# Kernel optimization log

Hardware: AMD Instinct MI355X
Metric: run time of the kernel (lower is better)

The kernel has to match this reference:

```python
import jax, jax.numpy as jnp
import numpy as np

B, H, F, E, K = 32, 4096, 4096, 8, 2

def setup_inputs() -> dict:
    key = jax.random.key(0)
    ks = jax.random.split(key, 5)
    x = jax.random.normal(ks[0], (B, H), dtype=jnp.float32)
    Wg = jax.random.normal(ks[1], (H, E), dtype=jnp.float32) * 0.02
    W1 = jax.random.normal(ks[2], (E, H, F), dtype=jnp.float32) * 0.02
    W3 = jax.random.normal(ks[3], (E, H, F), dtype=jnp.float32) * 0.02
    W2 = jax.random.normal(ks[4], (E, F, H), dtype=jnp.float32) * 0.02
    return {"x": x, "Wg": Wg, "W1": W1, "W3": W3, "W2": W2}

def reference(x, Wg, W1, W3, W2):
    # Gate: [B, E] logits, top-2 selection, softmax over the 2 selected logits
    logits = x @ Wg                                   # [B, E]
    vals, idx = jax.lax.top_k(logits, K)              # [B, K]
    w = jax.nn.softmax(vals, axis=-1)                 # [B, K]
    # Combine weights per expert: [B, E] (zero for unselected experts)
    combine = jnp.sum(jax.nn.one_hot(idx, E, dtype=x.dtype) * w[..., None], axis=1)
    h = jnp.einsum('bh,ehf->ebf', x, W1)              # [E, B, F]
    g = jax.nn.silu(h) * jnp.einsum('bh,ehf->ebf', x, W3)
    y = jnp.einsum('ebf,efh->ebh', g, W2)             # [E, B, H]
    # Scatter-combine: weighted sum over experts (all-gather + reduce-sum in source)
    return jnp.einsum('be,ebh->bh', combine, y)       # [B, H]
```

## Files before the change

kernel.cpp:

```cpp
#include <hip/hip_runtime.h>
#include <cstdint>

#define BB 32
#define HH 4096
#define FF 4096
#define EE 8
#define NSLOT 16
#define TSEG 16

__global__ __launch_bounds__(256) void gate_kernel(const float* __restrict__ x,
                                                   const float* __restrict__ Wg,
                                                   float* __restrict__ logits) {
  int b = blockIdx.x;
  int tid = threadIdx.x;
  float acc[EE];
#pragma unroll
  for (int e = 0; e < EE; ++e) acc[e] = 0.f;
  const float* xb = x + (size_t)b * HH;
  for (int h = tid; h < HH; h += 256) {
    float xv = xb[h];
    const float4* wg = (const float4*)(Wg + (size_t)h * EE);
    float4 w0 = wg[0], w1 = wg[1];
    acc[0] = fmaf(xv, w0.x, acc[0]);
    acc[1] = fmaf(xv, w0.y, acc[1]);
    acc[2] = fmaf(xv, w0.z, acc[2]);
    acc[3] = fmaf(xv, w0.w, acc[3]);
    acc[4] = fmaf(xv, w1.x, acc[4]);
    acc[5] = fmaf(xv, w1.y, acc[5]);
    acc[6] = fmaf(xv, w1.z, acc[6]);
    acc[7] = fmaf(xv, w1.w, acc[7]);
  }
#pragma unroll
  for (int off = 32; off > 0; off >>= 1) {
#pragma unroll
    for (int e = 0; e < EE; ++e) acc[e] += __shfl_down(acc[e], off, 64);
  }
  __shared__ float part[4][EE];
  if ((tid & 63) == 0) {
#pragma unroll
    for (int e = 0; e < EE; ++e) part[tid >> 6][e] = acc[e];
  }
  __syncthreads();
  if (tid < EE) {
    logits[(size_t)b * EE + tid] =
        part[0][tid] + part[1][tid] + part[2][tid] + part[3][tid];
  }
}

__global__ void route_kernel(const float* __restrict__ logits,
                             int* __restrict__ cnt,
                             int* __restrict__ tok,
                             float* __restrict__ wts,
                             int* __restrict__ ord) {
  if (threadIdx.x != 0 || blockIdx.x != 0) return;
  int e0[BB], e1[BB];
  float p0[BB], p1[BB];
  for (int b = 0; b < BB; ++b) {
    const float* L = logits + (size_t)b * EE;
    int i0 = 0;
    float v0 = L[0];
    for (int e = 1; e < EE; ++e) {
      float v = L[e];
      if (v > v0) { v0 = v; i0 = e; }
    }
    int i1 = (i0 == 0) ? 1 : 0;
    float v1 = L[i1];
    for (int e = 0; e < EE; ++e) {
      if (e == i0) continue;
      float v = L[e];
      if (v > v1) { v1 = v; i1 = e; }
    }
    float p = 1.f / (1.f + __expf(v1 - v0));
    e0[b] = i0; e1[b] = i1; p0[b] = p; p1[b] = 1.f - p;
  }
  for (int s = 0; s < NSLOT; ++s) {
    cnt[s] = 0;
    for (int t = 0; t < TSEG; ++t) { tok[s * TSEG + t] = 0; wts[s * TSEG + t] = 0.f; }
  }
  for (int e = 0; e < EE; ++e) {
    int c = 0;
    for (int b = 0; b < BB; ++b) {
      float w = 0.f;
      int sel = 0;
      if (e0[b] == e) { w = p0[b]; sel = 1; }
      else if (e1[b] == e) { w = p1[b]; sel = 1; }
      if (sel) {
        int s = e * 2 + (c >> 4);
        int t = c & 15;
        tok[s * TSEG + t] = b;
        wts[s * TSEG + t] = w;
        cnt[s] = t + 1;
        ++c;
      }
    }
  }
  int na = 0;
  for (int s = 0; s < NSLOT; ++s) if (cnt[s] > 0) ord[na++] = s;
  for (int s = 0; s < NSLOT; ++s) if (cnt[s] == 0) ord[na++] = s;
}

__global__ __launch_bounds__(256) void buildx_kernel(const float* __restrict__ x,
                                                     const int* __restrict__ cnt,
                                                     const int* __restrict__ tok,
                                                     float* __restrict__ xseg) {
  int s = blockIdx.y;
  int c = cnt[s];
  if (c == 0) return;
  int tid = threadIdx.x;
  int t = tid & 15;
  int hoff = tid >> 4;
  int tk = tok[s * TSEG + t];
  bool act = t < c;
  int hbase = blockIdx.x * 256;
#pragma unroll
  for (int i = 0; i < 16; ++i) {
    int h = hbase + i * 16 + hoff;
    float v = act ? x[(size_t)tk * HH + h] : 0.f;
    xseg[((size_t)s * HH + h) * TSEG + t] = v;
  }
}

template <int NT>
__device__ __forceinline__ void fma_row2(float2* __restrict__ acc,
                                         const float* __restrict__ xr, float2 wv) {
  float xs[NT];
#pragma unroll
  for (int q = 0; q < NT; q += 4) *(float4*)&xs[q] = *(const float4*)(xr + q);
#pragma unroll
  for (int t = 0; t < NT; ++t) {
    acc[t].x = fmaf(xs[t], wv.x, acc[t].x);
    acc[t].y = fmaf(xs[t], wv.y, acc[t].y);
  }
}

template <int NT>
__device__ __forceinline__ void accum256_f2(float2* __restrict__ acc,
                                            const float* __restrict__ wp,
                                            const float* __restrict__ xr) {
  float2 ring[16];
#pragma unroll
  for (int k = 0; k < 16; ++k) ring[k] = *(const float2*)(wp + (size_t)k * 4096);
  for (int i0 = 0; i0 + 16 < 256; i0 += 16) {
#pragma unroll
    for (int k = 0; k < 16; ++k) {
      float2 wv = ring[k];
      ring[k] = *(const float2*)(wp + (size_t)(i0 + 16 + k) * 4096);
      fma_row2<NT>(acc, xr + (size_t)(i0 + k) * NT, wv);
    }
  }
#pragma unroll
  for (int k = 0; k < 16; ++k)
    fma_row2<NT>(acc, xr + (size_t)(240 + k) * NT, ring[k]);
}

template <int NT>
__device__ __forceinline__ void stageT(float* __restrict__ lx,
                                       const float* __restrict__ src, int tid) {
  const float4* s4 = (const float4*)src;
  float4* d4 = (float4*)lx;
#pragma unroll
  for (int k = 0; k < NT; ++k) {
    int q = k * 256 + tid;
    int row = q / (NT / 4);
    int part = q & ((NT / 4) - 1);
    d4[q] = s4[row * 4 + part];
  }
}

template <int NT>
__device__ __forceinline__ void stage_silu(float* __restrict__ lx,
                                           const float* __restrict__ h1p,
                                           const float* __restrict__ h3p, int tid) {
  const float4* a4 = (const float4*)h1p;
  const float4* b4 = (const float4*)h3p;
  float4* d4 = (float4*)lx;
#pragma unroll
  for (int k = 0; k < NT; ++k) {
    int q = k * 256 + tid;
    int row = q / (NT / 4);
    int part = q & ((NT / 4) - 1);
    float4 a = a4[row * 4 + part];
    float4 b = b4[row * 4 + part];
    float4 g;
    g.x = (a.x / (1.f + __expf(-a.x))) * b.x;
    g.y = (a.y / (1.f + __expf(-a.y))) * b.y;
    g.z = (a.z / (1.f + __expf(-a.z))) * b.z;
    g.w = (a.w / (1.f + __expf(-a.w))) * b.w;
    d4[q] = g;
  }
}

template <int NT>
__device__ __forceinline__ void passB_body(const float* __restrict__ Wm,
                                           const float* __restrict__ xsrc,
                                           float* __restrict__ segbase,
                                           float* __restrict__ lx, int tid) {
  int l = tid & 63;
  int w = tid >> 6;
  float2 acc[NT];
#pragma unroll
  for (int t = 0; t < NT; ++t) acc[t] = make_float2(0.f, 0.f);
  for (int ch = 0; ch < 4; ++ch) {
    __syncthreads();
    stageT<NT>(lx, xsrc + (size_t)(ch * 1024) * TSEG, tid);
    __syncthreads();
    accum256_f2<NT>(acc, Wm + (size_t)(ch * 1024 + w * 256) * FF + 2 * l,
                    lx + (size_t)(w * 256) * NT);
  }
  __syncthreads();
  float2* red = (float2*)lx;
#pragma unroll
  for (int t = 0; t < NT; ++t) red[(t * 4 + w) * 64 + l] = acc[t];
  __syncthreads();
  constexpr int TH = NT / 2;
  int col_off = tid & 127;
  int half = tid >> 7;
  int lp = col_off >> 1;
  int comp = col_off & 1;
  float v[TH];
#pragma unroll
  for (int j = 0; j < TH; ++j) {
    int t = half * TH + j;
    float sum = 0.f;
#pragma unroll
    for (int w4 = 0; w4 < 4; ++w4)
      sum += lx[(((t * 4 + w4) * 64 + lp) << 1) + comp];
    v[j] = sum;
  }
  float* seg = segbase + (size_t)col_off * TSEG + half * TH;
#pragma unroll
  for (int q = 0; q < TH; q += 4) *(float4*)(seg + q) = *(const float4*)&v[q];
}

__global__ __launch_bounds__(256) void passB6_kernel(const float* __restrict__ W1,
                                                     const float* __restrict__ W3,
                                                     const float* __restrict__ xseg,
                                                     float* __restrict__ h1seg,
                                                     float* __restrict__ h3seg,
                                                     const int* __restrict__ cnt,
                                                     const int* __restrict__ ord) {
  __shared__ float lx[1024 * TSEG];
  int gy = blockIdx.y;
  int s = ord[gy >> 1];
  int mat = gy & 1;
  int c = cnt[s];
  if (c == 0) return;
  int e = s >> 1;
  int colbase = blockIdx.x * 128;
  const float* Wm = (mat ? W3 : W1) + (size_t)e * HH * FF + colbase;
  const float* xsrc = xseg + (size_t)s * HH * TSEG;
  float* segbase = (mat ? h3seg : h1seg) + ((size_t)s * FF + colbase) * TSEG;
  if (c <= 8)
    passB_body<8>(Wm, xsrc, segbase, lx, threadIdx.x);
  else
    passB_body<16>(Wm, xsrc, segbase, lx, threadIdx.x);
}

template <int NT>
__device__ __forceinline__ void passC_body(const float* __restrict__ Wm,
                                           const float* __restrict__ h1src,
                                           const float* __restrict__ h3src,
                                           float* __restrict__ out,
                                           const int* __restrict__ stok,
                                           const float* __restrict__ swt,
                                           int c, int colbase,
                                           float* __restrict__ lx, int tid) {
  int l = tid & 63;
  int w = tid >> 6;
  float2 acc[NT];
#pragma unroll
  for (int t = 0; t < NT; ++t) acc[t] = make_float2(0.f, 0.f);
  for (int ch = 0; ch < 2; ++ch) {
    __syncthreads();
    stage_silu<NT>(lx, h1src + (size_t)(ch * 1024) * TSEG,
                   h3src + (size_t)(ch * 1024) * TSEG, tid);
    __syncthreads();
    accum256_f2<NT>(acc, Wm + (size_t)(ch * 1024 + w * 256) * HH + 2 * l,
                    lx + (size_t)(w * 256) * NT);
  }
  __syncthreads();
  float2* red = (float2*)lx;
#pragma unroll
  for (int t = 0; t < NT; ++t) red[(t * 4 + w) * 64 + l] = acc[t];
  __syncthreads();
  constexpr int TH = NT / 2;
  int col_off = tid & 127;
  int half = tid >> 7;
  int lp = col_off >> 1;
  int comp = col_off & 1;
  float* op = out + colbase + col_off;
#pragma unroll
  for (int j = 0; j < TH; ++j) {
    int t = half * TH + j;
    if (t < c) {
      float sum = 0.f;
#pragma unroll
      for (int w4 = 0; w4 < 4; ++w4)
        sum += lx[(((t * 4 + w4) * 64 + lp) << 1) + comp];
      atomicAdd(op + (size_t)stok[t] * HH, swt[t] * sum);
    }
  }
}

__global__ __launch_bounds__(256) void passC6_kernel(const float* __restrict__ W2,
                                                     const float* __restrict__ h1seg,
                                                     const float* __restrict__ h3seg,
                                                     const int* __restrict__ cnt,
                                                     const int* __restrict__ tok,
                                                     const float* __restrict__ wts,
                                                     const int* __restrict__ ord,
                                                     float* __restrict__ out) {
  __shared__ float lx[1024 * TSEG];
  __shared__ int stok[TSEG];
  __shared__ float swt[TSEG];
  int gy = blockIdx.y;
  int s = ord[gy >> 1];
  int z = gy & 1;
  int c = cnt[s];
  if (c == 0) return;
  int e = s >> 1;
  int colbase = blockIdx.x * 128;
  if (threadIdx.x < TSEG) {
    stok[threadIdx.x] = tok[s * TSEG + threadIdx.x];
    swt[threadIdx.x] = wts[s * TSEG + threadIdx.x];
  }
  const float* Wm = W2 + (size_t)e * FF * HH + (size_t)(z * 2048) * HH + colbase;
  const float* h1src = h1seg + ((size_t)s * FF + z * 2048) * TSEG;
  const float* h3src = h3seg + ((size_t)s * FF + z * 2048) * TSEG;
  if (c <= 8)
    passC_body<8>(Wm, h1src, h3src, out, stok, swt, c, colbase, lx, threadIdx.x);
  else
    passC_body<16>(Wm, h1src, h3src, out, stok, swt, c, colbase, lx, threadIdx.x);
}

extern "C" void kernel_launch(void* const* d_in, const int* in_sizes, int n_in,
                              void* d_out, int out_size, void* d_ws, size_t ws_size,
                              hipStream_t stream) {
  const float* x  = (const float*)d_in[0];
  const float* Wg = (const float*)d_in[1];
  const float* W1 = (const float*)d_in[2];
  const float* W3 = (const float*)d_in[3];
  const float* W2 = (const float*)d_in[4];
  float* out = (float*)d_out;

  char* ws = (char*)d_ws;
  float* logits = (float*)ws;
  int*   cnt    = (int*)(ws + 1024);
  int*   tok    = (int*)(ws + 1088);
  float* wts    = (float*)(ws + 2112);
  int*   ord    = (int*)(ws + 3136);
  float* xseg   = (float*)(ws + 4096);
  float* h1seg  = xseg + (size_t)NSLOT * HH * TSEG;
  float* h3seg  = h1seg + (size_t)NSLOT * FF * TSEG;

  hipMemsetAsync(d_out, 0, (size_t)out_size * sizeof(float), stream);
  gate_kernel<<<BB, 256, 0, stream>>>(x, Wg, logits);
  route_kernel<<<1, 64, 0, stream>>>(logits, cnt, tok, wts, ord);
  buildx_kernel<<<dim3(HH / 256, NSLOT), 256, 0, stream>>>(x, cnt, tok, xseg);
  passB6_kernel<<<dim3(FF / 128, NSLOT * 2), 256, 0, stream>>>(W1, W3, xseg, h1seg, h3seg, cnt, ord);
  passC6_kernel<<<dim3(HH / 128, NSLOT * 2), 256, 0, stream>>>(W2, h1seg, h3seg, cnt, tok, wts, ord, out);
}
```

Measured before the change: 403.2 us.

## Retile expert GEMV passes to float4 weight loads and split token halves

Rewrites the W1/W3 and W2 passes so each thread loads float4 (4 columns) of weights and handles 8 tokens, with lanes split into two token halves. Staging chunks shrink from 1024 to 512 rows, so LDS use drops and more blocks can be resident per CU. The cross-wave reduction now goes through a padded LDS layout (stride 36) to avoid bank conflicts. The c<=8 specialization is dropped, so slots with few tokens now always compute 16 token lanes, but the wider weight loads are meant to improve memory throughput on this bandwidth-bound workload.

```diff
diff --git a/kernel.cpp b/kernel.cpp
--- a/kernel.cpp
+++ b/kernel.cpp
@@ -7,6 +7,8 @@
 #define EE 8
 #define NSLOT 16
 #define TSEG 16
+#define CH 512
+#define RSTR 36
 
 __global__ __launch_bounds__(256) void gate_kernel(const float* __restrict__ x,
                                                    const float* __restrict__ Wg,
@@ -120,189 +122,143 @@
   }
 }
 
-template <int NT>
-__device__ __forceinline__ void fma_row2(float2* __restrict__ acc,
-                                         const float* __restrict__ xr, float2 wv) {
-  float xs[NT];
-#pragma unroll
-  for (int q = 0; q < NT; q += 4) *(float4*)&xs[q] = *(const float4*)(xr + q);
-#pragma unroll
-  for (int t = 0; t < NT; ++t) {
+__device__ __forceinline__ void fma8(float4* __restrict__ acc,
+                                     const float* __restrict__ xr, float4 wv) {
+  float xs[8];
+  *(float4*)&xs[0] = *(const float4*)(xr);
+  *(float4*)&xs[4] = *(const float4*)(xr + 4);
+#pragma unroll
+  for (int t = 0; t < 8; ++t) {
     acc[t].x = fmaf(xs[t], wv.x, acc[t].x);
     acc[t].y = fmaf(xs[t], wv.y, acc[t].y);
-  }
-}
-
-template <int NT>
-__device__ __forceinline__ void accum256_f2(float2* __restrict__ acc,
-                                            const float* __restrict__ wp,
-                                            const float* __restrict__ xr) {
-  float2 ring[16];
-#pragma unroll
-  for (int k = 0; k < 16; ++k) ring[k] = *(const float2*)(wp + (size_t)k * 4096);
-  for (int i0 = 0; i0 + 16 < 256; i0 += 16) {
-#pragma unroll
-    for (int k = 0; k < 16; ++k) {
-      float2 wv = ring[k];
-      ring[k] = *(const float2*)(wp + (size_t)(i0 + 16 + k) * 4096);
-      fma_row2<NT>(acc, xr + (size_t)(i0 + k) * NT, wv);
+    acc[t].z = fmaf(xs[t], wv.z, acc[t].z);
+    acc[t].w = fmaf(xs[t], wv.w, acc[t].w);
+  }
+}
+
+__device__ __forceinline__ void accum128(float4* __restrict__ acc,
+                                         const float4* __restrict__ wp4,
+                                         const float* __restrict__ lxw,
+                                         int half8) {
+  float4 ring[8];
+#pragma unroll
+  for (int k = 0; k < 8; ++k) ring[k] = wp4[(size_t)k * 1024];
+  for (int i0 = 0; i0 + 8 < 128; i0 += 8) {
+#pragma unroll
+    for (int k = 0; k < 8; ++k) {
+      float4 wv = ring[k];
+      ring[k] = wp4[(size_t)(i0 + 8 + k) * 1024];
+      fma8(acc, lxw + (i0 + k) * TSEG + half8, wv);
     }
   }
 #pragma unroll
-  for (int k = 0; k < 16; ++k)
-    fma_row2<NT>(acc, xr + (size_t)(240 + k) * NT, ring[k]);
-}
-
-template <int NT>
-__device__ __forceinline__ void stageT(float* __restrict__ lx,
-                                       const float* __restrict__ src, int tid) {
+  for (int k = 0; k < 8; ++k)
+    fma8(acc, lxw + (120 + k) * TSEG + half8, ring[k]);
+}
+
+__device__ __forceinline__ void stage512(float* __restrict__ lx,
+                                         const float* __restrict__ src, int tid) {
   const float4* s4 = (const float4*)src;
   float4* d4 = (float4*)lx;
 #pragma unroll
-  for (int k = 0; k < NT; ++k) {
-    int q = k * 256 + tid;
-    int row = q / (NT / 4);
-    int part = q & ((NT / 4) - 1);
-    d4[q] = s4[row * 4 + part];
-  }
-}
-
-template <int NT>
-__device__ __forceinline__ void stage_silu(float* __restrict__ lx,
-                                           const float* __restrict__ h1p,
-                                           const float* __restrict__ h3p, int tid) {
+  for (int k = 0; k < 8; ++k) d4[k * 256 + tid] = s4[k * 256 + tid];
+}
+
+__device__ __forceinline__ void stage_silu512(float* __restrict__ lx,
+                                              const float* __restrict__ h1p,
+                                              const float* __restrict__ h3p, int tid) {
   const float4* a4 = (const float4*)h1p;
   const float4* b4 = (const float4*)h3p;
   float4* d4 = (float4*)lx;
 #pragma unroll
-  for (int k = 0; k < NT; ++k) {
-    int q = k * 256 + tid;
-    int row = q / (NT / 4);
-    int part = q & ((NT / 4) - 1);
-    float4 a = a4[row * 4 + part];
-    float4 b = b4[row * 4 + part];
+  for (int k = 0; k < 8; ++k) {
+    float4 a = a4[k * 256 + tid];
+    float4 b = b4[k * 256 + tid];
     float4 g;
     g.x = (a.x / (1.f + __expf(-a.x))) * b.x;
     g.y = (a.y / (1.f + __expf(-a.y))) * b.y;
     g.z = (a.z / (1.f + __expf(-a.z))) * b.z;
     g.w = (a.w / (1.f + __expf(-a.w))) * b.w;
-    d4[q] = g;
-  }
-}
-
-template <int NT>
-__device__ __forceinline__ void passB_body(const float* __restrict__ Wm,
-                                           const float* __restrict__ xsrc,
-                                           float* __restrict__ segbase,
-                                           float* __restrict__ lx, int tid) {
+    d4[k * 256 + tid] = g;
+  }
+}
+
+__device__ __forceinline__ void red_write(float* __restrict__ lds,
+                                          const float4* __restrict__ acc, int tid) {
   int l = tid & 63;
   int w = tid >> 6;
-  float2 acc[NT];
-#pragma unroll
-  for (int t = 0; t < NT; ++t) acc[t] = make_float2(0.f, 0.f);
-  for (int ch = 0; ch < 4; ++ch) {
-    __syncthreads();
-    stageT<NT>(lx, xsrc + (size_t)(ch * 1024) * TSEG, tid);
-    __syncthreads();
-    accum256_f2<NT>(acc, Wm + (size_t)(ch * 1024 + w * 256) * FF + 2 * l,
-                    lx + (size_t)(w * 256) * NT);
-  }
-  __syncthreads();
-  float2* red = (float2*)lx;
-#pragma unroll
-  for (int t = 0; t < NT; ++t) red[(t * 4 + w) * 64 + l] = acc[t];
-  __syncthreads();
-  constexpr int TH = NT / 2;
-  int col_off = tid & 127;
+  float tmp[32];
+#pragma unroll
+  for (int t = 0; t < 8; ++t) {
+    tmp[t] = acc[t].x;
+    tmp[8 + t] = acc[t].y;
+    tmp[16 + t] = acc[t].z;
+    tmp[24 + t] = acc[t].w;
+  }
+  float* rp = lds + (size_t)(w * 64 + l) * RSTR;
+#pragma unroll
+  for (int q = 0; q < 32; q += 4) *(float4*)(rp + q) = *(const float4*)&tmp[q];
+}
+
+__device__ __forceinline__ void red_read(const float* __restrict__ lds,
+                                         float* __restrict__ v, int tid) {
+  int col = tid & 127;
   int half = tid >> 7;
-  int lp = col_off >> 1;
-  int comp = col_off & 1;
-  float v[TH];
-#pragma unroll
-  for (int j = 0; j < TH; ++j) {
-    int t = half * TH + j;
+  int base = (half * 32 + (col >> 2)) * RSTR + (col & 3) * 8;
+#pragma unroll
+  for (int t = 0; t < 8; ++t) {
     float sum = 0.f;
 #pragma unroll
-    for (int w4 = 0; w4 < 4; ++w4)
-      sum += lx[(((t * 4 + w4) * 64 + lp) << 1) + comp];
-    v[j] = sum;
-  }
-  float* seg = segbase + (size_t)col_off * TSEG + half * TH;
-#pragma unroll
-  for (int q = 0; q < TH; q += 4) *(float4*)(seg + q) = *(const float4*)&v[q];
-}
-
-__global__ __launch_bounds__(256) void passB6_kernel(const float* __restrict__ W1,
+    for (int w = 0; w < 4; ++w) sum += lds[w * 64 * RSTR + base + t];
+    v[t] = sum;
+  }
+}
+
+__global__ __launch_bounds__(256) void passB7_kernel(const float* __restrict__ W1,
                                                      const float* __restrict__ W3,
                                                      const float* __restrict__ xseg,
                                                      float* __restrict__ h1seg,
                                                      float* __restrict__ h3seg,
                                                      const int* __restrict__ cnt,
                                                      const int* __restrict__ ord) {
-  __shared__ float lx[1024 * TSEG];
+  __shared__ float lds[4 * 64 * RSTR];
   int gy = blockIdx.y;
   int s = ord[gy >> 1];
   int mat = gy & 1;
   int c = cnt[s];
   if (c == 0) return;
   int e = s >> 1;
-  int colbase = blockIdx.x * 128;
-  const float* Wm = (mat ? W3 : W1) + (size_t)e * HH * FF + colbase;
-  const float* xsrc = xseg + (size_t)s * HH * TSEG;
-  float* segbase = (mat ? h3seg : h1seg) + ((size_t)s * FF + colbase) * TSEG;
-  if (c <= 8)
-    passB_body<8>(Wm, xsrc, segbase, lx, threadIdx.x);
-  else
-    passB_body<16>(Wm, xsrc, segbase, lx, threadIdx.x);
-}
-
-template <int NT>
-__device__ __forceinline__ void passC_body(const float* __restrict__ Wm,
-                                           const float* __restrict__ h1src,
-                                           const float* __restrict__ h3src,
-                                           float* __restrict__ out,
-                                           const int* __restrict__ stok,
-                                           const float* __restrict__ swt,
-                                           int c, int colbase,
-                                           float* __restrict__ lx, int tid) {
+  int tid = threadIdx.x;
   int l = tid & 63;
   int w = tid >> 6;
-  float2 acc[NT];
-#pragma unroll
-  for (int t = 0; t < NT; ++t) acc[t] = make_float2(0.f, 0.f);
-  for (int ch = 0; ch < 2; ++ch) {
+  int colbase = blockIdx.x * 128;
+  const float* Wm = (mat ? W3 : W1) + (size_t)e * HH * FF + colbase + (l & 31) * 4;
+  const float* xsrc = xseg + (size_t)s * HH * TSEG;
+  int half8 = (l >> 5) * 8;
+  float4 acc[8];
+#pragma unroll
+  for (int t = 0; t < 8; ++t) acc[t] = make_float4(0.f, 0.f, 0.f, 0.f);
+  for (int ch = 0; ch < HH / CH; ++ch) {
     __syncthreads();
-    stage_silu<NT>(lx, h1src + (size_t)(ch * 1024) * TSEG,
-                   h3src + (size_t)(ch * 1024) * TSEG, tid);
+    stage512(lds, xsrc + (size_t)(ch * CH) * TSEG, tid);
     __syncthreads();
-    accum256_f2<NT>(acc, Wm + (size_t)(ch * 1024 + w * 256) * HH + 2 * l,
-                    lx + (size_t)(w * 256) * NT);
-  }
-  __syncthreads();
-  float2* red = (float2*)lx;
-#pragma unroll
-  for (int t = 0; t < NT; ++t) red[(t * 4 + w) * 64 + l] = acc[t];
-  __syncthreads();
-  constexpr int TH = NT / 2;
-  int col_off = tid & 127;
+    const float4* wp4 = (const float4*)(Wm + (size_t)(ch * CH + w * 128) * FF);
+    accum128(acc, wp4, lds + (w * 128) * TSEG, half8);
+  }
+  __syncthreads();
+  red_write(lds, acc, tid);
+  __syncthreads();
+  float v[8];
+  red_read(lds, v, tid);
+  int col = tid & 127;
   int half = tid >> 7;
-  int lp = col_off >> 1;
-  int comp = col_off & 1;
-  float* op = out + colbase + col_off;
-#pragma unroll
-  for (int j = 0; j < TH; ++j) {
-    int t = half * TH + j;
-    if (t < c) {
-      float sum = 0.f;
-#pragma unroll
-      for (int w4 = 0; w4 < 4; ++w4)
-        sum += lx[(((t * 4 + w4) * 64 + lp) << 1) + comp];
-      atomicAdd(op + (size_t)stok[t] * HH, swt[t] * sum);
-    }
-  }
-}
-
-__global__ __launch_bounds__(256) void passC6_kernel(const float* __restrict__ W2,
+  float* seg = (mat ? h3seg : h1seg) +
+               ((size_t)s * FF + colbase + col) * TSEG + half * 8;
+  *(float4*)(seg) = *(const float4*)&v[0];
+  *(float4*)(seg + 4) = *(const float4*)&v[4];
+}
+
+__global__ __launch_bounds__(256) void passC7_kernel(const float* __restrict__ W2,
                                                      const float* __restrict__ h1seg,
                                                      const float* __restrict__ h3seg,
                                                      const int* __restrict__ cnt,
@@ -310,7 +266,7 @@
                                                      const float* __restrict__ wts,
                                                      const int* __restrict__ ord,
                                                      float* __restrict__ out) {
-  __shared__ float lx[1024 * TSEG];
+  __shared__ float lds[4 * 64 * RSTR];
   __shared__ int stok[TSEG];
   __shared__ float swt[TSEG];
   int gy = blockIdx.y;
@@ -319,18 +275,43 @@
   int c = cnt[s];
   if (c == 0) return;
   int e = s >> 1;
+  int tid = threadIdx.x;
+  int l = tid & 63;
+  int w = tid >> 6;
   int colbase = blockIdx.x * 128;
-  if (threadIdx.x < TSEG) {
-    stok[threadIdx.x] = tok[s * TSEG + threadIdx.x];
-    swt[threadIdx.x] = wts[s * TSEG + threadIdx.x];
-  }
-  const float* Wm = W2 + (size_t)e * FF * HH + (size_t)(z * 2048) * HH + colbase;
+  if (tid < TSEG) {
+    stok[tid] = tok[s * TSEG + tid];
+    swt[tid] = wts[s * TSEG + tid];
+  }
+  const float* Wm = W2 + (size_t)e * FF * HH + (size_t)(z * 2048) * HH +
+                    colbase + (l & 31) * 4;
   const float* h1src = h1seg + ((size_t)s * FF + z * 2048) * TSEG;
   const float* h3src = h3seg + ((size_t)s * FF + z * 2048) * TSEG;
-  if (c <= 8)
-    passC_body<8>(Wm, h1src, h3src, out, stok, swt, c, colbase, lx, threadIdx.x);
-  else
-    passC_body<16>(Wm, h1src, h3src, out, stok, swt, c, colbase, lx, threadIdx.x);
+  int half8 = (l >> 5) * 8;
+  float4 acc[8];
+#pragma unroll
+  for (int t = 0; t < 8; ++t) acc[t] = make_float4(0.f, 0.f, 0.f, 0.f);
+  for (int ch = 0; ch < 4; ++ch) {
+    __syncthreads();
+    stage_silu512(lds, h1src + (size_t)(ch * CH) * TSEG,
+                  h3src + (size_t)(ch * CH) * TSEG, tid);
+    __syncthreads();
+    const float4* wp4 = (const float4*)(Wm + (size_t)(ch * CH + w * 128) * HH);
+    accum128(acc, wp4, lds + (w * 128) * TSEG, half8);
+  }
+  __syncthreads();
+  red_write(lds, acc, tid);
+  __syncthreads();
+  float v[8];
+  red_read(lds, v, tid);
+  int col = tid & 127;
+  int half = tid >> 7;
+  float* op = out + colbase + col;
+#pragma unroll
+  for (int t = 0; t < 8; ++t) {
+    int tt = half * 8 + t;
+    if (tt < c) atomicAdd(op + (size_t)stok[tt] * HH, swt[tt] * v[t]);
+  }
 }
 
 extern "C" void kernel_launch(void* const* d_in, const int* in_sizes, int n_in,
@@ -357,6 +338,6 @@
   gate_kernel<<<BB, 256, 0, stream>>>(x, Wg, logits);
   route_kernel<<<1, 64, 0, stream>>>(logits, cnt, tok, wts, ord);
   buildx_kernel<<<dim3(HH / 256, NSLOT), 256, 0, stream>>>(x, cnt, tok, xseg);
-  passB6_kernel<<<dim3(FF / 128, NSLOT * 2), 256, 0, stream>>>(W1, W3, xseg, h1seg, h3seg, cnt, ord);
-  passC6_kernel<<<dim3(HH / 128, NSLOT * 2), 256, 0, stream>>>(W2, h1seg, h3seg, cnt, tok, wts, ord, out);
-}
+  passB7_kernel<<<dim3(FF / 128, NSLOT * 2), 256, 0, stream>>>(W1, W3, xseg, h1seg, h3seg, cnt, ord);
+  passC7_kernel<<<dim3(HH / 128, NSLOT * 2), 256, 0, stream>>>(W2, h1seg, h3seg, cnt, tok, wts, ord, out);
+}
```

Result: faster. 362.3 us (-10.1%).
